# Performance work log

Measured on AMD Instinct MI355X. Metric: run time of the kernel, lower is better.

Reference implementation:

```python
import jax, jax.numpy as jnp
import numpy as np
from jax import lax

STRIDE = 16
OFFSET = 8.0  # vgg16 backbone
C = 512
A = 9  # 3 ratios x 3 scales
THR = 0.05
IOU_THR = 0.7
N_OUT = 50
K = 2048  # fixed candidate budget for jit-able NMS

# anchors: rows of [[1,1],[1,2],[2,1]] * scale for scale in (128,256,512) -> [9,2] (w,h)
ANCHORS = np.concatenate([np.array([[1, 1], [1, 2], [2, 1]], np.float32) * s
                          for s in (128.0, 256.0, 512.0)], axis=0)


def _conv(x, w, b, pad):
    y = lax.conv_general_dilated(x, w, (1, 1), [(pad, pad), (pad, pad)],
                                 dimension_numbers=("NCHW", "OIHW", "NCHW"))
    return y + b[None, :, None, None]


def setup_inputs() -> dict:
    key = jax.random.key(0)
    ks = jax.random.split(key, 8)
    x = jax.random.normal(ks[0], (4, C, 64, 96), dtype=jnp.float32)
    w1 = jax.random.normal(ks[1], (C, C, 3, 3), dtype=jnp.float32) * 0.02
    b1 = jnp.zeros((C,), jnp.float32)
    w_cls = jax.random.normal(ks[2], (2 * A, C, 1, 1), dtype=jnp.float32) * 0.02
    b_cls = jnp.zeros((2 * A,), jnp.float32)
    w_reg = jax.random.normal(ks[3], (4 * A, C, 1, 1), dtype=jnp.float32) * 0.02
    b_reg = jnp.zeros((4 * A,), jnp.float32)
    return {"x": x, "w1": w1, "b1": b1, "w_cls": w_cls, "b_cls": b_cls,
            "w_reg": w_reg, "b_reg": b_reg, "h": 1024, "w": 1536}


def _rpn_forward(x, w1, b1, w_cls, b_cls, w_reg, b_reg, h, w):
    B = x.shape[0]
    f = _conv(x, w1, b1, 1)                      # [B,512,H,W] (no activation in original)
    cls = _conv(f, w_cls, b_cls, 0)              # [B,2A,H,W]
    cls = jax.nn.softmax(cls, axis=1)            # Softmax2d: over ALL 2A channels
    reg = _conv(f, w_reg, b_reg, 0)              # [B,4A,H,W]
    H, W = cls.shape[-2:]
    prob_fg = cls.reshape(B, A, 2, H, W)[:, :, 1]           # [B,A,H,W]
    reg = reg.reshape(B, A, 4, H, W).transpose(0, 1, 3, 4, 2)  # [B,A,H,W,4]

    scores = prob_fg.reshape(-1)                  # [B*A*H*W]
    reg_flat = reg.reshape(-1, 4)

    # threshold (torch.where) -> fixed-size top-K preselection for jit
    masked = jnp.where(scores >= THR, scores, -1.0)
    top_s, top_i = lax.top_k(masked, K)          # sorted descending
    valid = top_s >= THR

    # recover (a, y, x) from flat index; batch index is dropped (as in original NMS)
    aidx = (top_i // (H * W)) % A
    yidx = (top_i // W) % H
    xidx = top_i % W

    off_x = (w - OFFSET * 2) % STRIDE / 2 + OFFSET
    off_y = (h - OFFSET * 2) % STRIDE / 2 + OFFSET
    cx = xidx.astype(jnp.float32) * STRIDE + off_x
    cy = yidx.astype(jnp.float32) * STRIDE + off_y
    anc = jnp.asarray(ANCHORS)[aidx]             # [K,2] (w,h)

    r = reg_flat[top_i]                          # [K,4]
    bx = r[:, 0] * anc[:, 0] + cx
    by = r[:, 1] * anc[:, 1] + cy
    bw = jnp.exp(r[:, 2]) * anc[:, 0]
    bh = jnp.exp(r[:, 3]) * anc[:, 1]
    x1 = bx - bw * 0.5
    y1 = by - bh * 0.5
    x2 = bx + bw * 0.5
    y2 = by + bh * 0.5
    boxes = jnp.stack([x1, y1, x2, y2], axis=1)  # [K,4] xyxy

    # pairwise IoU [K,K]
    area = (x2 - x1) * (y2 - y1)
    ix1 = jnp.maximum(x1[:, None], x1[None, :])
    iy1 = jnp.maximum(y1[:, None], y1[None, :])
    ix2 = jnp.minimum(x2[:, None], x2[None, :])
    iy2 = jnp.minimum(y2[:, None], y2[None, :])
    inter = jnp.clip(ix2 - ix1, 0.0) * jnp.clip(iy2 - iy1, 0.0)
    iou = inter / (area[:, None] + area[None, :] - inter + 1e-9)

    idx = jnp.arange(K)

    def body(i, keep):
        sup = keep[i] & (iou[i] > IOU_THR) & (idx > i)
        return keep & ~sup

    keep = lax.fori_loop(0, K, body, valid)

    final_s = jnp.where(keep, top_s, -1.0)
    sel_s, sel_i = lax.top_k(final_s, N_OUT)     # first N kept, score order
    out_valid = sel_s >= THR
    out_scores = jnp.where(out_valid, sel_s, 0.0)
    out_boxes = jnp.where(out_valid[:, None], boxes[sel_i], 0.0)
    return out_scores, out_boxes


def reference(x, w1, b1, w_cls, b_cls, w_reg, b_reg, h, w):
    return _rpn_forward(x, w1, b1, w_cls, b_cls, w_reg, b_reg, h, w)
```

## Files before the change

kernel.cpp:

```cpp
#include <hip/hip_runtime.h>
#include <stdint.h>

#define NB 4
#define NC 512
#define NH 64
#define NW 96
#define NA 9
#define NPIX (NB*NA*NH*NW)
#define KSEL 2048
#define NOUT 50
#define THRS 0.05f

#define HIST_BASE 0x3D4CCu
#define HIST_SIZE 9024
#define CAND_CAP 8192

typedef _Float16 half8 __attribute__((ext_vector_type(8)));
typedef float floatx16 __attribute__((ext_vector_type(16)));

__device__ const float ANC_W[9] = {128.f,128.f,256.f,256.f,256.f,512.f,512.f,512.f,1024.f};
__device__ const float ANC_H[9] = {128.f,256.f,128.f,256.f,512.f,256.f,512.f,1024.f,512.f};

__global__ __launch_bounds__(256) void wexp2_k(const float* __restrict__ w1,
                                               uint4* __restrict__ wexp2) {
    __shared__ __align__(16) _Float16 lbuf[36 * 32 * 8];
    const int bid = blockIdx.x;
    const int cc = bid >> 4, cog = bid & 15;
    const int t = threadIdx.x;
    const int co_l = t >> 3, j = t & 7;
    const int co = cog * 32 + co_l;
    const float* r0 = w1 + ((size_t)co * 512 + cc * 16 + j) * 9;
    const float* r1 = r0 + 8 * 9;
#pragma unroll
    for (int kk = 0; kk < 9; ++kk) {
        const float v0 = r0[kk] * 1024.f;
        const float v1 = r1[kk] * 1024.f;
        const _Float16 h0 = (_Float16)v0, h1 = (_Float16)v1;
        const _Float16 l0 = (_Float16)(v0 - (float)h0);
        const _Float16 l1 = (_Float16)(v1 - (float)h1);
        lbuf[((kk * 4 + 0) * 32 + co_l) * 8 + j] = h0;
        lbuf[((kk * 4 + 1) * 32 + co_l) * 8 + j] = h1;
        lbuf[((kk * 4 + 2) * 32 + co_l) * 8 + j] = l0;
        lbuf[((kk * 4 + 3) * 32 + co_l) * 8 + j] = l1;
    }
    __syncthreads();
    for (int e = t; e < 1152; e += 256) {
        const int co_e = e & 31;
        const int rest = e >> 5;
        const int kk = rest >> 2, kd = rest & 3;
        const uint4 v = *(const uint4*)&lbuf[(rest * 32 + co_e) * 8];
        wexp2[(((size_t)(cc * 9 + kk) * 4 + kd) * 512) + cog * 32 + co_e] = v;
    }
}

#define XS_BYTES 12480
#define WB_BYTES 16384
#define CONV_LDS (XS_BYTES + 2*WB_BYTES)

__global__ __launch_bounds__(512, 4) void conv_mfma(
    const float* __restrict__ x, const uint4* __restrict__ wexp2,
    const float* __restrict__ b1, float* __restrict__ f)
{
    __shared__ __align__(16) char smem[CONV_LDS];
    char* xs = smem;
    char* wb = smem + XS_BYTES;
    const int t = threadIdx.x;
    const int bid = blockIdx.x;
    const int half = bid & 1, pxb = bid >> 1;
    const int b = pxb >> 6, r = pxb & 63, by = r >> 2, bx = r & 3;
    const int y0 = by * 4, x0 = bx * 24;
    const int wq = t >> 6, lane = t & 63;
    const int m32 = lane & 31, khalf = lane >> 5;

    int abase[3];
#pragma unroll
    for (int mt = 0; mt < 3; ++mt) {
        const int px = mt * 32 + m32;
        const int yl = px / 24, xl = px - yl * 24;
        abase[mt] = (yl * 26 + xl) * 80 + khalf * 16;
    }
    const int bb0 = (wq * 32 + m32) * 16 + khalf * 4096;

    floatx16 acc[3];
#pragma unroll
    for (int mt = 0; mt < 3; ++mt)
#pragma unroll
        for (int i = 0; i < 16; ++i) acc[mt][i] = 0.f;

    const int co_l = t & 255, pp = t >> 8;
    const uint4* wsrc = wexp2 + half * 256 + co_l;
    uint4 pf0, pf1;
    auto loadw = [&](int q2) {
        const size_t base = (size_t)q2 * 2048;
        pf0 = wsrc[base + (size_t)pp * 512];
        pf1 = wsrc[base + (size_t)(pp + 2) * 512];
    };
    const int wa0 = pp * 4096 + co_l * 16;
    const int wa1 = (pp + 2) * 4096 + co_l * 16;

    const float* xb = x + (size_t)b * NC * (NH * NW);
    auto stage_x = [&](int cc) {
        const float* xc = xb + (size_t)cc * 16 * (NH * NW);
        for (int it = t; it < 312; it += 512) {
            const int kh = (it >= 156) ? 1 : 0;
            const int slot = it - kh * 156;
            const int ya = slot / 26, xa = slot - ya * 26;
            const int gy = y0 - 1 + ya, gx = x0 - 1 + xa;
            const bool ok = (gy >= 0 && gy < NH && gx >= 0 && gx < NW);
            const int off = ok ? (kh * 8 * 6144 + gy * 96 + gx) : 0;
            union { _Float16 h[8]; uint4 u; } hi, lo;
#pragma unroll
            for (int j = 0; j < 8; ++j) {
                const float v = (ok ? xc[off + j * 6144] : 0.f) * 1024.f;
                const _Float16 hh = (_Float16)v;
                hi.h[j] = hh;
                lo.h[j] = (_Float16)(v - (float)hh);
            }
            *(uint4*)(xs + slot * 80 + kh * 16) = hi.u;
            *(uint4*)(xs + slot * 80 + 32 + kh * 16) = lo.u;
        }
    };

    loadw(0);
    *(uint4*)(wb + wa0) = pf0;
    *(uint4*)(wb + wa1) = pf1;
    loadw(1);

    int cc = 0, kk = 0;
    for (int q = 0; q < 288; ++q) {
        if (kk == 0) {
            __syncthreads();
            stage_x(cc);
        }
        __syncthreads();
        if (q < 287) {
            char* wd = wb + ((q + 1) & 1) * WB_BYTES;
            *(uint4*)(wd + wa0) = pf0;
            *(uint4*)(wd + wa1) = pf1;
            if (q < 286) loadw(q + 2);
        }
        {
            const int ky = kk / 3, kx = kk - ky * 3;
            const char* xcur = xs + (ky * 26 + kx) * 80;
            half8 axh[3], axl[3];
#pragma unroll
            for (int mt = 0; mt < 3; ++mt) {
                axh[mt] = *(const half8*)(xcur + abase[mt]);
                axl[mt] = *(const half8*)(xcur + abase[mt] + 32);
            }
            const char* wc = wb + (q & 1) * WB_BYTES + bb0;
            const half8 bwh = *(const half8*)(wc);
            const half8 bwl = *(const half8*)(wc + 8192);
#pragma unroll
            for (int mt = 0; mt < 3; ++mt)
                acc[mt] = __builtin_amdgcn_mfma_f32_32x32x16_f16(
                    axh[mt], bwh, acc[mt], 0, 0, 0);
#pragma unroll
            for (int mt = 0; mt < 3; ++mt)
                acc[mt] = __builtin_amdgcn_mfma_f32_32x32x16_f16(
                    axh[mt], bwl, acc[mt], 0, 0, 0);
#pragma unroll
            for (int mt = 0; mt < 3; ++mt)
                acc[mt] = __builtin_amdgcn_mfma_f32_32x32x16_f16(
                    axl[mt], bwh, acc[mt], 0, 0, 0);
        }
        if (++kk == 9) { kk = 0; ++cc; }
    }

    const float inv = 1.0f / 1048576.0f;
    const int co = half * 256 + wq * 32 + m32;
    const float bias = b1[co];
#pragma unroll
    for (int mt = 0; mt < 3; ++mt) {
#pragma unroll
        for (int reg = 0; reg < 16; ++reg) {
            const int row = (reg & 3) + 8 * (reg >> 2) + 4 * khalf;
            const int pxl = mt * 32 + row;
            const int yl = pxl / 24, xl = pxl - yl * 24;
            const size_t gpx = (size_t)(b * 64 + y0 + yl) * 96 + (x0 + xl);
            f[gpx * 512 + co] = acc[mt][reg] * inv + bias;
        }
    }
}

__global__ __launch_bounds__(256) void head_k(
    const float* __restrict__ f, const float* __restrict__ wcls,
    const float* __restrict__ wreg, const float* __restrict__ bcls,
    const float* __restrict__ breg, float* __restrict__ scores,
    float* __restrict__ regs)
{
    __shared__ __align__(16) float smem[6912 + 128 * 57];
    float* wls = smem;
    float* lt  = smem + 6912;
    const int t = threadIdx.x;
    const int px0 = blockIdx.x * 128;
    const int px_l = t & 127, oh = t >> 7;
    float acc27[27];
#pragma unroll
    for (int k = 0; k < 27; ++k) acc27[k] = 0.f;

    for (int qd = 0; qd < 4; ++qd) {
        __syncthreads();
        for (int e = t; e < 6912; e += 256) {
            const int oc = e >> 7, c = e & 127;
            wls[e] = (oc < 18) ? wcls[oc * 512 + qd * 128 + c]
                               : wreg[(oc - 18) * 512 + qd * 128 + c];
        }
        __syncthreads();
        const float4* fp = (const float4*)(f + (size_t)(px0 + px_l) * 512 + qd * 128);
        const float4* wp4 = (const float4*)wls;
#pragma unroll 4
        for (int c4 = 0; c4 < 32; ++c4) {
            const float4 fv = fp[c4];
#pragma unroll
            for (int k = 0; k < 27; ++k) {
                const float4 wv = wp4[(oh * 27 + k) * 32 + c4];
                acc27[k] += fv.x * wv.x + fv.y * wv.y + fv.z * wv.z + fv.w * wv.w;
            }
        }
    }
    __syncthreads();
#pragma unroll
    for (int k = 0; k < 27; ++k) lt[px_l * 57 + oh * 27 + k] = acc27[k];
    __syncthreads();

    if (t < 128) {
        const int px = px0 + t;
        const float* row = lt + t * 57;
        float cl[18];
        float m = -1e30f;
#pragma unroll
        for (int oc = 0; oc < 18; ++oc) {
            cl[oc] = row[oc] + bcls[oc];
            m = fmaxf(m, cl[oc]);
        }
        float sum = 0.f;
#pragma unroll
        for (int oc = 0; oc < 18; ++oc) { cl[oc] = expf(cl[oc] - m); sum += cl[oc]; }
        const float inv = 1.f / sum;
        const int b = px / 6144;
        const int yx = px - b * 6144;
#pragma unroll
        for (int a = 0; a < 9; ++a) {
            const int idx = b * 55296 + a * 6144 + yx;
            scores[idx] = cl[2 * a + 1] * inv;
            float4 rv;
            rv.x = row[18 + a * 4 + 0] + breg[a * 4 + 0];
            rv.y = row[18 + a * 4 + 1] + breg[a * 4 + 1];
            rv.z = row[18 + a * 4 + 2] + breg[a * 4 + 2];
            rv.w = row[18 + a * 4 + 3] + breg[a * 4 + 3];
            ((float4*)regs)[idx] = rv;
        }
    }
}

__global__ void hist_k(const float* __restrict__ scores, uint32_t* __restrict__ hist) {
    const int i = blockIdx.x * 256 + threadIdx.x;
    const float s = scores[i];
    if (s >= THRS) {
        int bkt = (int)(__float_as_uint(s) >> 12) - (int)HIST_BASE;
        bkt = min(max(bkt, 0), HIST_SIZE - 1);
        atomicAdd(&hist[bkt], 1u);
    }
}

__global__ void scan_k(const uint32_t* __restrict__ hist, uint32_t* __restrict__ ctl) {
    __shared__ uint32_t ssum[1024];
    const int t = threadIdx.x;
    uint32_t s = 0;
#pragma unroll
    for (int u = 0; u < 9; ++u) {
        const int bkt = t * 9 + u;
        if (bkt < HIST_SIZE) s += hist[bkt];
    }
    const uint32_t mysum = s;
    ssum[t] = s;
    __syncthreads();
    for (int off = 1; off < 1024; off <<= 1) {
        uint32_t v = (t + off < 1024) ? ssum[t + off] : 0u;
        __syncthreads();
        ssum[t] += v;
        __syncthreads();
    }
    const uint32_t total = ssum[0];
    const uint32_t above = (t < 1023) ? ssum[t + 1] : 0u;
    if (total < KSEL) {
        if (t == 0) ctl[0] = HIST_BASE;
    } else if (above < KSEL && above + mysum >= KSEL) {
        uint32_t run = above;
        for (int u = 8; u >= 0; --u) {
            const int bkt = t * 9 + u;
            if (bkt >= HIST_SIZE) continue;
            run += hist[bkt];
            if (run >= KSEL) { ctl[0] = HIST_BASE + (uint32_t)bkt; break; }
        }
    }
}

__global__ void collect_k(const float* __restrict__ scores, uint32_t* __restrict__ ctl,
                          uint64_t* __restrict__ cand) {
    const int i = blockIdx.x * 256 + threadIdx.x;
    const float s = scores[i];
    if (s >= THRS) {
        const uint32_t bits = __float_as_uint(s);
        if ((bits >> 12) >= ctl[0]) {
            const uint32_t pos = atomicAdd(&ctl[1], 1u);
            if (pos < CAND_CAP)
                cand[pos] = ((uint64_t)bits << 32) | (uint64_t)(0xFFFFFFFFu - (uint32_t)i);
        }
    }
}

__global__ void sort_decode_k(const uint64_t* __restrict__ cand, const uint32_t* __restrict__ ctl,
                              const float* __restrict__ regs,
                              const int* __restrict__ hp, const int* __restrict__ wp,
                              float* __restrict__ tops_s, float* __restrict__ boxes) {
    __shared__ uint64_t keys[CAND_CAP];
    const int t = threadIdx.x;
    const int M = min((int)ctl[1], CAND_CAP);
    const int N = (M <= 4096) ? 4096 : 8192;
    for (int k = t; k < N; k += 1024) keys[k] = (k < M) ? cand[k] : 0ull;
    __syncthreads();
    for (int size = 2; size <= N; size <<= 1) {
        for (int stride = size >> 1; stride > 0; stride >>= 1) {
            for (int k = t; k < N; k += 1024) {
                const int p = k ^ stride;
                if (p > k) {
                    const uint64_t a = keys[k], bb = keys[p];
                    const bool sw = ((k & size) == 0) ? (a < bb) : (a > bb);
                    if (sw) { keys[k] = bb; keys[p] = a; }
                }
            }
            __syncthreads();
        }
    }
    const int w_in = wp[0], h_in = hp[0];
    const float offx = (float)((w_in - 16) % 16) * 0.5f + 8.0f;
    const float offy = (float)((h_in - 16) % 16) * 0.5f + 8.0f;
    for (int k = t; k < KSEL; k += 1024) {
        const uint64_t key = keys[k];
        float sc = -1.f, x1 = 0.f, y1 = 0.f, x2 = 0.f, y2 = 0.f;
        if (k < M && key != 0ull) {
            const uint32_t idx = 0xFFFFFFFFu - (uint32_t)(key & 0xFFFFFFFFull);
            sc = __uint_as_float((uint32_t)(key >> 32));
            const int a  = (int)(idx / (NH * NW)) % NA;
            const int yy = (int)(idx / NW) % NH;
            const int xx = (int)(idx % NW);
            const float4 r = ((const float4*)regs)[idx];
            const float aw = ANC_W[a], ah = ANC_H[a];
            const float cx = (float)xx * 16.f + offx;
            const float cy = (float)yy * 16.f + offy;
            const float bx = r.x * aw + cx;
            const float by = r.y * ah + cy;
            const float bw = expf(r.z) * aw;
            const float bh = expf(r.w) * ah;
            x1 = bx - bw * 0.5f; y1 = by - bh * 0.5f;
            x2 = bx + bw * 0.5f; y2 = by + bh * 0.5f;
        }
        tops_s[k] = sc;
        ((float4*)boxes)[k] = make_float4(x1, y1, x2, y2);
    }
}

__global__ void iou_k(const float* __restrict__ boxes, uint64_t* __restrict__ mask) {
    __shared__ float4 jb[64];
    const int t = threadIdx.x;
    const int bi = blockIdx.x, bj = blockIdx.y;
    jb[t] = ((const float4*)boxes)[bj * 64 + t];
    __syncthreads();
    const int i = bi * 64 + t;
    const float4 mb = ((const float4*)boxes)[i];
    const float areai = (mb.z - mb.x) * (mb.w - mb.y);
    uint64_t w = 0;
    for (int jj = 0; jj < 64; ++jj) {
        const float4 ob = jb[jj];
        const int j = bj * 64 + jj;
        const float ix1 = fmaxf(mb.x, ob.x);
        const float iy1 = fmaxf(mb.y, ob.y);
        const float ix2 = fminf(mb.z, ob.z);
        const float iy2 = fminf(mb.w, ob.w);
        const float inter = fmaxf(ix2 - ix1, 0.f) * fmaxf(iy2 - iy1, 0.f);
        const float areaj = (ob.z - ob.x) * (ob.w - ob.y);
        const float iou = inter / (areai + areaj - inter + 1e-9f);
        if (iou > 0.7f && j > i) w |= (1ull << jj);
    }
    mask[(size_t)i * 32 + bj] = w;
}

__global__ void nms_k(const float* __restrict__ tops_s, const float* __restrict__ boxes,
                      const uint64_t* __restrict__ mask, float* __restrict__ out) {
    __shared__ uint64_t remv[32];
    __shared__ float ssc[KSEL];
    __shared__ int sel[NOUT];
    const int t = threadIdx.x;
    for (int k = t; k < KSEL; k += 64) ssc[k] = tops_s[k];
    if (t < 32) remv[t] = 0ull;
    uint64_t nextrow = (t < 32) ? mask[t] : 0ull;
    int cnt = 0;
    for (int i = 0; i < KSEL && cnt < NOUT; ++i) {
        const uint64_t cur = nextrow;
        if (t < 32 && i + 1 < KSEL) nextrow = mask[(size_t)(i + 1) * 32 + t];
        const uint64_t rw = remv[i >> 6];
        const bool sup = (rw >> (i & 63)) & 1ull;
        if (ssc[i] >= THRS && !sup) {
            if (t < 32) remv[t] |= cur;
            if (t == 0) sel[cnt] = i;
            ++cnt;
        }
    }
    for (int k = t; k < NOUT; k += 64) {
        float s = 0.f;
        float4 bb = make_float4(0.f, 0.f, 0.f, 0.f);
        if (k < cnt) { const int i = sel[k]; s = ssc[i]; bb = ((const float4*)boxes)[i]; }
        out[k] = s;
        out[NOUT + k * 4 + 0] = bb.x;
        out[NOUT + k * 4 + 1] = bb.y;
        out[NOUT + k * 4 + 2] = bb.z;
        out[NOUT + k * 4 + 3] = bb.w;
    }
}

extern "C" void kernel_launch(void* const* d_in, const int* in_sizes, int n_in,
                              void* d_out, int out_size, void* d_ws, size_t ws_size,
                              hipStream_t stream) {
    const float* x    = (const float*)d_in[0];
    const float* w1   = (const float*)d_in[1];
    const float* b1   = (const float*)d_in[2];
    const float* wcls = (const float*)d_in[3];
    const float* bcls = (const float*)d_in[4];
    const float* wreg = (const float*)d_in[5];
    const float* breg = (const float*)d_in[6];
    const int*   hp   = (const int*)d_in[7];
    const int*   wp   = (const int*)d_in[8];
    float* out = (float*)d_out;

    char* ws = (char*)d_ws;
    size_t off = 0;
    auto carve = [&](size_t bytes) -> void* {
        void* p = ws + off;
        off = (off + bytes + 255) & ~(size_t)255;
        return p;
    };
    uint4*    wexp2  = (uint4*)carve((size_t)288 * 4 * 512 * 16);
    float*    f      = (float*)carve((size_t)24576 * 512 * 4);
    float*    scores = (float*)carve((size_t)NPIX * 4);
    float*    regs   = (float*)carve((size_t)NPIX * 16);
    uint32_t* hist   = (uint32_t*)carve((size_t)HIST_SIZE * 4);
    uint32_t* ctl    = (uint32_t*)carve(256);
    uint64_t* cand   = (uint64_t*)carve((size_t)CAND_CAP * 8);
    float*    tops_s = (float*)carve((size_t)KSEL * 4);
    float*    boxes  = (float*)carve((size_t)KSEL * 16);
    uint64_t* mask   = (uint64_t*)carve((size_t)KSEL * 32 * 8);
    (void)ws_size; (void)in_sizes; (void)n_in; (void)out_size;

    hipMemsetAsync(hist, 0, (size_t)HIST_SIZE * 4, stream);
    hipMemsetAsync(ctl, 0, 256, stream);

    wexp2_k<<<512, 256, 0, stream>>>(w1, wexp2);
    conv_mfma<<<512, 512, 0, stream>>>(x, wexp2, b1, f);
    head_k<<<192, 256, 0, stream>>>(f, wcls, wreg, bcls, breg, scores, regs);
    hist_k<<<NPIX / 256, 256, 0, stream>>>(scores, hist);
    scan_k<<<1, 1024, 0, stream>>>(hist, ctl);
    collect_k<<<NPIX / 256, 256, 0, stream>>>(scores, ctl, cand);
    sort_decode_k<<<1, 1024, 0, stream>>>(cand, ctl, regs, hp, wp, tops_s, boxes);
    iou_k<<<dim3(KSEL / 64, KSEL / 64), 64, 0, stream>>>(boxes, mask);
    nms_k<<<1, 64, 0, stream>>>(tops_s, boxes, mask, out);
}
```

Measured before the change: 668.3 us.

## Load conv weights directly to registers and privatize histogram in LDS

The conv kernel no longer stages weight tiles through a double-buffered LDS area. Each lane now loads its B-operand fragments straight from global memory into registers, prefetching one step ahead, and the per-step barrier is kept only around x staging. This removes LDS traffic and one barrier per iteration, but each wave now issues its own global loads for weights and relies on cache hits. Separately, the histogram kernel reads four scores per thread with float4 loads, counts them with LDS atomics, then flushes nonzero bins to global memory, cutting contention on global atomics.

```diff
diff --git a/kernel.cpp b/kernel.cpp
--- a/kernel.cpp
+++ b/kernel.cpp
@@ -47,23 +47,19 @@
     for (int e = t; e < 1152; e += 256) {
         const int co_e = e & 31;
         const int rest = e >> 5;
-        const int kk = rest >> 2, kd = rest & 3;
         const uint4 v = *(const uint4*)&lbuf[(rest * 32 + co_e) * 8];
-        wexp2[(((size_t)(cc * 9 + kk) * 4 + kd) * 512) + cog * 32 + co_e] = v;
+        wexp2[(((size_t)cc * 9) * 4 + rest) * 512 + cog * 32 + co_e] = v;
     }
 }
 
 #define XS_BYTES 12480
-#define WB_BYTES 16384
-#define CONV_LDS (XS_BYTES + 2*WB_BYTES)
+#define CONV_LDS XS_BYTES
 
 __global__ __launch_bounds__(512, 4) void conv_mfma(
     const float* __restrict__ x, const uint4* __restrict__ wexp2,
     const float* __restrict__ b1, float* __restrict__ f)
 {
-    __shared__ __align__(16) char smem[CONV_LDS];
-    char* xs = smem;
-    char* wb = smem + XS_BYTES;
+    __shared__ __align__(16) char xs[CONV_LDS];
     const int t = threadIdx.x;
     const int bid = blockIdx.x;
     const int half = bid & 1, pxb = bid >> 1;
@@ -79,7 +75,6 @@
         const int yl = px / 24, xl = px - yl * 24;
         abase[mt] = (yl * 26 + xl) * 80 + khalf * 16;
     }
-    const int bb0 = (wq * 32 + m32) * 16 + khalf * 4096;
 
     floatx16 acc[3];
 #pragma unroll
@@ -87,16 +82,7 @@
 #pragma unroll
         for (int i = 0; i < 16; ++i) acc[mt][i] = 0.f;
 
-    const int co_l = t & 255, pp = t >> 8;
-    const uint4* wsrc = wexp2 + half * 256 + co_l;
-    uint4 pf0, pf1;
-    auto loadw = [&](int q2) {
-        const size_t base = (size_t)q2 * 2048;
-        pf0 = wsrc[base + (size_t)pp * 512];
-        pf1 = wsrc[base + (size_t)(pp + 2) * 512];
-    };
-    const int wa0 = pp * 4096 + co_l * 16;
-    const int wa1 = (pp + 2) * 4096 + co_l * 16;
+    const uint4* wsrc = wexp2 + (size_t)khalf * 512 + (half * 256 + wq * 32 + m32);
 
     const float* xb = x + (size_t)b * NC * (NH * NW);
     auto stage_x = [&](int cc) {
@@ -121,23 +107,21 @@
         }
     };
 
-    loadw(0);
-    *(uint4*)(wb + wa0) = pf0;
-    *(uint4*)(wb + wa1) = pf1;
-    loadw(1);
+    uint4 bch, bcl, bnh, bnl;
+    bch = wsrc[0];
+    bcl = wsrc[1024];
 
     int cc = 0, kk = 0;
     for (int q = 0; q < 288; ++q) {
         if (kk == 0) {
             __syncthreads();
             stage_x(cc);
-        }
-        __syncthreads();
+            __syncthreads();
+        }
         if (q < 287) {
-            char* wd = wb + ((q + 1) & 1) * WB_BYTES;
-            *(uint4*)(wd + wa0) = pf0;
-            *(uint4*)(wd + wa1) = pf1;
-            if (q < 286) loadw(q + 2);
+            const size_t nb = (size_t)(q + 1) * 2048;
+            bnh = wsrc[nb];
+            bnl = wsrc[nb + 1024];
         }
         {
             const int ky = kk / 3, kx = kk - ky * 3;
@@ -148,9 +132,8 @@
                 axh[mt] = *(const half8*)(xcur + abase[mt]);
                 axl[mt] = *(const half8*)(xcur + abase[mt] + 32);
             }
-            const char* wc = wb + (q & 1) * WB_BYTES + bb0;
-            const half8 bwh = *(const half8*)(wc);
-            const half8 bwl = *(const half8*)(wc + 8192);
+            const half8 bwh = __builtin_bit_cast(half8, bch);
+            const half8 bwl = __builtin_bit_cast(half8, bcl);
 #pragma unroll
             for (int mt = 0; mt < 3; ++mt)
                 acc[mt] = __builtin_amdgcn_mfma_f32_32x32x16_f16(
@@ -164,6 +147,7 @@
                 acc[mt] = __builtin_amdgcn_mfma_f32_32x32x16_f16(
                     axl[mt], bwh, acc[mt], 0, 0, 0);
         }
+        bch = bnh; bcl = bnl;
         if (++kk == 9) { kk = 0; ++cc; }
     }
 
@@ -254,13 +238,27 @@
     }
 }
 
-__global__ void hist_k(const float* __restrict__ scores, uint32_t* __restrict__ hist) {
-    const int i = blockIdx.x * 256 + threadIdx.x;
-    const float s = scores[i];
-    if (s >= THRS) {
-        int bkt = (int)(__float_as_uint(s) >> 12) - (int)HIST_BASE;
-        bkt = min(max(bkt, 0), HIST_SIZE - 1);
-        atomicAdd(&hist[bkt], 1u);
+__global__ __launch_bounds__(256) void hist_k(const float* __restrict__ scores,
+                                              uint32_t* __restrict__ hist) {
+    __shared__ uint32_t lh[HIST_SIZE];
+    const int t = threadIdx.x;
+    for (int e = t; e < HIST_SIZE; e += 256) lh[e] = 0u;
+    __syncthreads();
+    const float4 sv = ((const float4*)scores)[blockIdx.x * 256 + t];
+    const float s4[4] = {sv.x, sv.y, sv.z, sv.w};
+#pragma unroll
+    for (int j = 0; j < 4; ++j) {
+        const float s = s4[j];
+        if (s >= THRS) {
+            int bkt = (int)(__float_as_uint(s) >> 12) - (int)HIST_BASE;
+            bkt = min(max(bkt, 0), HIST_SIZE - 1);
+            atomicAdd(&lh[bkt], 1u);
+        }
+    }
+    __syncthreads();
+    for (int e = t; e < HIST_SIZE; e += 256) {
+        const uint32_t v = lh[e];
+        if (v) atomicAdd(&hist[e], v);
     }
 }
 
@@ -459,7 +457,7 @@
     wexp2_k<<<512, 256, 0, stream>>>(w1, wexp2);
     conv_mfma<<<512, 512, 0, stream>>>(x, wexp2, b1, f);
     head_k<<<192, 256, 0, stream>>>(f, wcls, wreg, bcls, breg, scores, regs);
-    hist_k<<<NPIX / 256, 256, 0, stream>>>(scores, hist);
+    hist_k<<<216, 256, 0, stream>>>(scores, hist);
     scan_k<<<1, 1024, 0, stream>>>(hist, ctl);
     collect_k<<<NPIX / 256, 256, 0, stream>>>(scores, ctl, cand);
     sort_decode_k<<<1, 1024, 0, stream>>>(cand, ctl, regs, hp, wp, tops_s, boxes);
```

After: 656.1 us. Within noise of the previous version (-1.8%).
